# Optimization experiments

Measured on AMD Instinct MI355X. Metric: run time of the kernel, lower is better.

The kernel has to match this reference:

```python
import jax, jax.numpy as jnp
import numpy as np

B, N, K = 32, 2048, 16          # graphs, nodes per graph, knn neighbors
F_IN, F_OUT, P = 32, 64, 3      # feature dims, pos dim


def setup_inputs() -> dict:
    key = jax.random.key(0)
    ks = jax.random.split(key, 6)
    x = jax.random.normal(ks[0], (B * N, F_IN), dtype=jnp.float32)
    pos = jax.random.normal(ks[1], (B * N, P), dtype=jnp.float32)
    # contiguous equal-size graphs: batch[i] = i // N
    batch = (jnp.arange(B * N, dtype=jnp.int32) // N).astype(jnp.int32)
    W_edge = jax.random.normal(ks[2], (2 * F_IN, F_OUT), dtype=jnp.float32) * 0.1
    b_edge = jax.random.normal(ks[3], (F_OUT,), dtype=jnp.float32) * 0.1
    W_nn = jax.random.normal(ks[4], (F_IN, F_OUT), dtype=jnp.float32) * 0.1
    b_nn = jax.random.normal(ks[5], (F_OUT,), dtype=jnp.float32) * 0.1
    return {"x": x, "pos": pos, "W_edge": W_edge, "b_edge": b_edge,
            "W_nn": W_nn, "b_nn": b_nn, "batch": batch}


def reference(x, pos, W_edge, b_edge, W_nn, b_nn, batch):
    # batch is contiguous with N nodes per graph -> reshape to [B, N, .]
    xb = x.reshape(B, N, F_IN)
    pb = pos.reshape(B, N, P)

    # --- knn_graph on pos, per graph (flow='source_to_target') ---
    sq = jnp.sum(pb * pb, axis=-1)                                   # [B, N]
    d2 = sq[:, :, None] + sq[:, None, :] - 2.0 * jnp.einsum('bnd,bmd->bnm', pb, pb)
    d2 = d2 + jnp.eye(N, dtype=d2.dtype) * 1e30                      # exclude self-loops
    _, idx = jax.lax.top_k(-d2, K)                                   # idx[b, i, k] = k-th nearest j of i

    # --- EdgeConv: message = edge_nn(concat(x_i, x_j - x_i)), aggr=max at i ---
    x_j = jnp.take_along_axis(xb, idx.reshape(B, N * K, 1), axis=1).reshape(B, N, K, F_IN)
    x_i = xb[:, :, None, :]                                          # [B, N, 1, F_IN]
    msg = jnp.concatenate([jnp.broadcast_to(x_i, (B, N, K, F_IN)), x_j - x_i], axis=-1)
    h = jax.nn.relu(msg @ W_edge + b_edge)                           # [B, N, K, F_OUT]
    edge_out = jnp.max(h, axis=2)                                    # max-aggregate over neighbors

    # --- skip branch: nn(x) ---
    skip = jax.nn.relu(xb @ W_nn + b_nn)                             # [B, N, F_OUT]

    return (edge_out + skip).reshape(B * N, F_OUT)
```

## Files before the change

kernel.cpp:

```cpp
#include <hip/hip_runtime.h>

#define NB     32
#define NPTS   2048
#define KNN    16
#define FIN    32
#define FOUT   64

typedef __attribute__((ext_vector_type(8))) short bf16x8;
typedef __attribute__((ext_vector_type(4))) float f32x4;

__device__ inline unsigned bf16pk(float lo, float hi) {
    unsigned a = __float_as_uint(lo), b = __float_as_uint(hi);
    a = (a + 0x7fffu + ((a >> 16) & 1u)) >> 16;
    b = (b + 0x7fffu + ((b >> 16) & 1u)) >> 16;
    return (a & 0xffffu) | (b << 16);
}


#define CEA(x, y) { float _t = fminf(x, y); y = fmaxf(x, y); x = _t; }
#define CED(x, y) { float _t = fmaxf(x, y); y = fminf(x, y); x = _t; }

#define BMERGE16(dk) \
    CEA(dk[0],dk[8])  CEA(dk[1],dk[9])  CEA(dk[2],dk[10]) CEA(dk[3],dk[11]) \
    CEA(dk[4],dk[12]) CEA(dk[5],dk[13]) CEA(dk[6],dk[14]) CEA(dk[7],dk[15]) \
    CEA(dk[0],dk[4])  CEA(dk[1],dk[5])  CEA(dk[2],dk[6])  CEA(dk[3],dk[7])  \
    CEA(dk[8],dk[12]) CEA(dk[9],dk[13]) CEA(dk[10],dk[14]) CEA(dk[11],dk[15]) \
    CEA(dk[0],dk[2])  CEA(dk[1],dk[3])  CEA(dk[4],dk[6])  CEA(dk[5],dk[7])  \
    CEA(dk[8],dk[10]) CEA(dk[9],dk[11]) CEA(dk[12],dk[14]) CEA(dk[13],dk[15]) \
    CEA(dk[0],dk[1])  CEA(dk[2],dk[3])  CEA(dk[4],dk[5])  CEA(dk[6],dk[7])  \
    CEA(dk[8],dk[9])  CEA(dk[10],dk[11]) CEA(dk[12],dk[13]) CEA(dk[14],dk[15])

#define NET8(a) \
    CED(a[0],a[1]) CED(a[2],a[3]) CED(a[4],a[5]) CED(a[6],a[7]) \
    CED(a[0],a[2]) CED(a[1],a[3]) CED(a[4],a[6]) CED(a[5],a[7]) \
    CED(a[1],a[2]) CED(a[5],a[6]) \
    CED(a[0],a[4]) CED(a[1],a[5]) CED(a[2],a[6]) CED(a[3],a[7]) \
    CED(a[2],a[4]) CED(a[3],a[5]) \
    CED(a[1],a[2]) CED(a[3],a[4]) CED(a[5],a[6])

__global__ __launch_bounds__(256) void sq_kernel(
    const float* __restrict__ pos, float4* __restrict__ P4)
{
    const int i = blockIdx.x * 256 + threadIdx.x;
    const float px = pos[i*3 + 0];
    const float py = pos[i*3 + 1];
    const float pz = pos[i*3 + 2];
    const float sq = __fadd_rn(__fadd_rn(__fmul_rn(px,px), __fmul_rn(py,py)),
                               __fmul_rn(pz,pz));
    P4[i] = make_float4(px, py, pz, sq);
}

#define CH   8
#define CHL  (NPTS / CH)

#define D2P(C, DST)                                                        \
    {                                                                      \
        float _dot = __fmaf_rn(me.z, (C).z,                                \
                      __fmaf_rn(me.y, (C).y, __fmul_rn(me.x, (C).x)));     \
        DST = __fmaf_rn(-2.0f, _dot, (C).w);                               \
    }

#define SBATCH2(JB, EXCLF)                                                 \
    {                                                                      \
        float a[8], a2[8];                                                 \
        _Pragma("unroll")                                                  \
        for (int i = 0; i < 8; ++i) {                                      \
            const int j = (JB) + i;                                        \
            const float4 c = pb4[j];                                       \
            float d2;                                                      \
            D2P(c, d2)                                                     \
            a[i] = (EXCLF && j == q) ? 1e30f : d2;                         \
        }                                                                  \
        _Pragma("unroll")                                                  \
        for (int i = 0; i < 8; ++i) {                                      \
            const int j = (JB) + 8 + i;                                    \
            const float4 c = pb4[j];                                       \
            float d2;                                                      \
            D2P(c, d2)                                                     \
            a2[i] = (EXCLF && j == q) ? 1e30f : d2;                        \
        }                                                                  \
        NET8(a)                                                            \
        NET8(a2)                                                           \
        _Pragma("unroll")                                                  \
        for (int i = 0; i < 8; ++i) dk[8+i] = fminf(dk[8+i], a[i]);        \
        BMERGE16(dk)                                                       \
        _Pragma("unroll")                                                  \
        for (int i = 0; i < 8; ++i) dk[8+i] = fminf(dk[8+i], a2[i]);       \
        BMERGE16(dk)                                                       \
    }

#define APP(DD, JJ)                                                        \
    if ((DD) <= tthr) {                                                    \
        if ((DD) < tthr) {                                                 \
            if (cntS + cntT >= KNN) --cntT;                                \
            JL[base + cntS * 64 + l] = (JJ);                               \
            ++cntS;                                                        \
        } else if (cntS + cntT < KNN) {                                    \
            JL[base + (KNN - 1 - cntT) * 64 + l] = (JJ);                   \
            ++cntT;                                                        \
        }                                                                  \
    }

#define RESC(JJ, EXCLF)                                                    \
    {                                                                      \
        const float4 c = pb4[(JJ)];                                        \
        float d2;                                                          \
        D2P(c, d2)                                                         \
        if (EXCLF && (JJ) == q) d2 = 1e30f;                                \
        APP(d2, (JJ))                                                      \
    }

#define ESTRIDE 66
#define IDXS    17

__global__ __launch_bounds__(512, 8) void knn_mlp_kernel(
    const float4* __restrict__ P4, const float* __restrict__ x,
    const float* __restrict__ W_edge, const float* __restrict__ b_edge,
    const float* __restrict__ W_nn,   const float* __restrict__ b_nn,
    float* __restrict__ out)
{
    __shared__ __attribute__((aligned(16))) char smem[39168];
    float* V    = (float*)smem;
    int*   CNTS = (int*)(smem + 32768);
    int*   IDX  = (int*)(smem + 34816);

    const int orig = blockIdx.x;
    const int b    = ((orig & 7) << 2) | ((orig >> 3) & 3);
    const int slab = orig >> 5;
    const int t    = threadIdx.x;
    const int w    = __builtin_amdgcn_readfirstlane(t >> 6);
    const int l    = t & 63;

    const float4* __restrict__ pb4 = P4 + (size_t)b * NPTS;
    const int    q  = slab * 64 + l;
    const float4 me = pb4[q];

    {
        float dk[KNN];
        #pragma unroll
        for (int s = 0; s < KNN; ++s) dk[s] = 1e30f;

        const int j0  = w * CHL;
        const int exw = slab >> 2;
        const int lo  = j0 + (slab & 3) * 64;

        if (w == exw) {
            for (int jb = j0;      jb < lo;        jb += 16) SBATCH2(jb, false)
            for (int jb = lo;      jb < lo + 64;   jb += 16) SBATCH2(jb, true)
            for (int jb = lo + 64; jb < j0 + CHL;  jb += 16) SBATCH2(jb, false)
        } else {
            for (int jb = j0;      jb < j0 + CHL;  jb += 16) SBATCH2(jb, false)
        }

        #pragma unroll
        for (int s = 0; s < KNN; ++s)
            V[(w * KNN + s) * 64 + l] = dk[s];
        __syncthreads();

        for (int c2 = 0; c2 < CH; ++c2) {
            if (c2 == w) continue;
            float v[KNN];
            #pragma unroll
            for (int s2 = 0; s2 < KNN; ++s2)
                v[s2] = V[(c2 * KNN + s2) * 64 + l];
            #pragma unroll
            for (int s = 0; s < KNN; ++s) dk[s] = fminf(dk[s], v[KNN-1-s]);
            BMERGE16(dk)
        }
        const float tthr = dk[KNN-1];
        __syncthreads();

        int* JL = (int*)V;
        const int base = w * KNN * 64;
        int cntS = 0, cntT = 0;
        if (w == exw) {
            for (int j = j0;      j < lo;        ++j) RESC(j, false)
            for (int j = lo;      j < lo + 64;   ++j) RESC(j, true)
            for (int j = lo + 64; j < j0 + CHL;  ++j) RESC(j, false)
        } else {
            for (int j = j0;      j < j0 + CHL;  ++j) RESC(j, false)
        }
        CNTS[w * 64 + l] = cntS | (cntT << 16);
        __syncthreads();

        if (w == 0) {
            int outc = 0;
            for (int c2 = 0; c2 < CH; ++c2) {
                int cs = CNTS[c2 * 64 + l] & 0xffff;
                for (int s2 = 0; s2 < cs && outc < KNN; ++s2)
                    IDX[l * IDXS + outc++] = JL[(c2 * KNN + s2) * 64 + l];
            }
            for (int c2 = 0; c2 < CH && outc < KNN; ++c2) {
                int ct = CNTS[c2 * 64 + l] >> 16;
                for (int s2 = 0; s2 < ct && outc < KNN; ++s2)
                    IDX[l * IDXS + outc++] =
                        JL[(c2 * KNN + (KNN - 1 - s2)) * 64 + l];
            }
        }
        __syncthreads();
    }

    const int c15 = l & 15;
    const int g   = l >> 4;
    const int nbase = b * NPTS + slab * 64;
    const int gbase = b * NPTS;

    float* E = (float*)smem;
    float* S = (float*)(smem + 16896);

    const f32x4 zf = {0.f, 0.f, 0.f, 0.f};

    {
        const int ng = w & 3;
        const int f0 = (w >> 2) * 2;

        const float* rp = x + (size_t)(nbase + ng * 16 + c15) * FIN + g * 8;
        float4 v0 = *(const float4*)rp;
        float4 v1 = *(const float4*)(rp + 4);
        int4 pk = make_int4(bf16pk(v0.x, v0.y), bf16pk(v0.z, v0.w),
                            bf16pk(v1.x, v1.y), bf16pk(v1.z, v1.w));
        bf16x8 afi = *(bf16x8*)&pk;

        #pragma unroll
        for (int ff = 0; ff < 2; ++ff) {
            const int col = 16 * (f0 + ff) + c15;
            unsigned pd[4], pn[4];
            #pragma unroll
            for (int d = 0; d < 4; ++d) {
                const int k0 = g * 8 + 2 * d;
                float h0 = W_edge[(FIN + k0)     * FOUT + col];
                float h1 = W_edge[(FIN + k0 + 1) * FOUT + col];
                pd[d] = bf16pk(W_edge[k0       * FOUT + col] - h0,
                               W_edge[(k0 + 1) * FOUT + col] - h1);
                pn[d] = bf16pk(W_nn[k0 * FOUT + col], W_nn[(k0+1) * FOUT + col]);
            }
            int4 bd = make_int4(pd[0], pd[1], pd[2], pd[3]);
            int4 bn = make_int4(pn[0], pn[1], pn[2], pn[3]);
            f32x4 baseF = __builtin_amdgcn_mfma_f32_16x16x32_bf16(
                afi, *(bf16x8*)&bd, zf, 0, 0, 0);
            f32x4 skipF = __builtin_amdgcn_mfma_f32_16x16x32_bf16(
                afi, *(bf16x8*)&bn, zf, 0, 0, 0);
            const float be  = b_edge[col];
            const float bnn = b_nn[col];
            #pragma unroll
            for (int reg = 0; reg < 4; ++reg) {
                const int nd = ng * 16 + g * 4 + reg;
                E[nd * ESTRIDE + col] = baseF[reg] + be;
                S[nd * ESTRIDE + col] = fmaxf(skipF[reg] + bnn, 0.f);
            }
        }
    }
    __syncthreads();

    {
        const int n0l = w * 8;

        int4 Bhi[4];
        #pragma unroll
        for (int ff = 0; ff < 4; ++ff) {
            const int col = 16 * ff + c15;
            unsigned ph[4];
            #pragma unroll
            for (int d = 0; d < 4; ++d) {
                const int k0 = g * 8 + 2 * d;
                ph[d] = bf16pk(W_edge[(FIN + k0)     * FOUT + col],
                               W_edge[(FIN + k0 + 1) * FOUT + col]);
            }
            Bhi[ff] = make_int4(ph[0], ph[1], ph[2], ph[3]);
        }

        int nbA = IDX[(n0l + 0) * IDXS + c15];
        int nbB = IDX[(n0l + 1) * IDXS + c15];
        const float* rpA = x + (size_t)(gbase + nbA) * FIN + g * 8;
        const float* rpB = x + (size_t)(gbase + nbB) * FIN + g * 8;
        float4 Aa = *(const float4*)rpA, Ab = *(const float4*)(rpA + 4);
        float4 Ba = *(const float4*)rpB, Bb = *(const float4*)(rpB + 4);

        #pragma unroll 1
        for (int i = 0; i < 8; i += 2) {
            float4 c0 = Aa, c1 = Ab;
            if (i + 2 < 8) {
                int nb = IDX[(n0l + i + 2) * IDXS + c15];
                const float* rp2 = x + (size_t)(gbase + nb) * FIN + g * 8;
                Aa = *(const float4*)rp2;
                Ab = *(const float4*)(rp2 + 4);
            }
            {
                int4 pk2 = make_int4(bf16pk(c0.x, c0.y), bf16pk(c0.z, c0.w),
                                     bf16pk(c1.x, c1.y), bf16pk(c1.z, c1.w));
                bf16x8 af = *(bf16x8*)&pk2;
                float rmax[4];
                #pragma unroll
                for (int ff = 0; ff < 4; ++ff) {
                    f32x4 z = __builtin_amdgcn_mfma_f32_16x16x32_bf16(
                        af, *(bf16x8*)&Bhi[ff], zf, 0, 0, 0);
                    float m = fmaxf(fmaxf(z[0], z[1]), fmaxf(z[2], z[3]));
                    m = fmaxf(m, __shfl_xor(m, 16));
                    m = fmaxf(m, __shfl_xor(m, 32));
                    rmax[ff] = m;
                }
                float val = (g == 0) ? rmax[0] : (g == 1) ? rmax[1]
                          : (g == 2) ? rmax[2] : rmax[3];
                const int nd = n0l + i;
                float e = fmaxf(val + E[nd * ESTRIDE + g * 16 + c15], 0.f);
                float s = S[nd * ESTRIDE + g * 16 + c15];
                out[(size_t)(nbase + nd) * FOUT + g * 16 + c15] = e + s;
            }

            float4 d0 = Ba, d1 = Bb;
            if (i + 3 < 8) {
                int nb = IDX[(n0l + i + 3) * IDXS + c15];
                const float* rp2 = x + (size_t)(gbase + nb) * FIN + g * 8;
                Ba = *(const float4*)rp2;
                Bb = *(const float4*)(rp2 + 4);
            }
            {
                int4 pk2 = make_int4(bf16pk(d0.x, d0.y), bf16pk(d0.z, d0.w),
                                     bf16pk(d1.x, d1.y), bf16pk(d1.z, d1.w));
                bf16x8 af = *(bf16x8*)&pk2;
                float rmax[4];
                #pragma unroll
                for (int ff = 0; ff < 4; ++ff) {
                    f32x4 z = __builtin_amdgcn_mfma_f32_16x16x32_bf16(
                        af, *(bf16x8*)&Bhi[ff], zf, 0, 0, 0);
                    float m = fmaxf(fmaxf(z[0], z[1]), fmaxf(z[2], z[3]));
                    m = fmaxf(m, __shfl_xor(m, 16));
                    m = fmaxf(m, __shfl_xor(m, 32));
                    rmax[ff] = m;
                }
                float val = (g == 0) ? rmax[0] : (g == 1) ? rmax[1]
                          : (g == 2) ? rmax[2] : rmax[3];
                const int nd = n0l + i + 1;
                float e = fmaxf(val + E[nd * ESTRIDE + g * 16 + c15], 0.f);
                float s = S[nd * ESTRIDE + g * 16 + c15];
                out[(size_t)(nbase + nd) * FOUT + g * 16 + c15] = e + s;
            }
        }
    }
}

extern "C" void kernel_launch(void* const* d_in, const int* in_sizes, int n_in,
                              void* d_out, int out_size, void* d_ws, size_t ws_size,
                              hipStream_t stream) {
    const float* x      = (const float*)d_in[0];
    const float* pos    = (const float*)d_in[1];
    const float* W_edge = (const float*)d_in[2];
    const float* b_edge = (const float*)d_in[3];
    const float* W_nn   = (const float*)d_in[4];
    const float* b_nn   = (const float*)d_in[5];

    float4* P4   = (float4*)d_ws;
    float*  outp = (float*)d_out;

    sq_kernel     <<<NB * NPTS / 256, 256, 0, stream>>>(pos, P4);
    knn_mlp_kernel<<<NB * 32,         512, 0, stream>>>(P4, x, W_edge, b_edge,
                                                        W_nn, b_nn, outp);
}
```

Baseline: 196.2 us.

## Software-pipeline candidate loads in KNN scans and parallelize index compaction across waves

Both the top-k scan and the rescan loop now prefetch the next 16 candidate positions into registers while the current batch is being processed, and the three-segment self-exclusion loops are merged into one uniform loop with a predicated check. The serial compaction of neighbor indices, previously done by wave 0 alone, is replaced by a per-wave prefix-sum placement so all 8 waves write their survivors in parallel. This is meant to hide global/L2 load latency and remove a serialized tail, at the cost of 16 extra float4 registers per thread, which may lower occupancy under the 512x8 launch bounds.

```diff
diff --git a/kernel.cpp b/kernel.cpp
--- a/kernel.cpp
+++ b/kernel.cpp
@@ -60,35 +60,6 @@
         DST = __fmaf_rn(-2.0f, _dot, (C).w);                               \
     }
 
-#define SBATCH2(JB, EXCLF)                                                 \
-    {                                                                      \
-        float a[8], a2[8];                                                 \
-        _Pragma("unroll")                                                  \
-        for (int i = 0; i < 8; ++i) {                                      \
-            const int j = (JB) + i;                                        \
-            const float4 c = pb4[j];                                       \
-            float d2;                                                      \
-            D2P(c, d2)                                                     \
-            a[i] = (EXCLF && j == q) ? 1e30f : d2;                         \
-        }                                                                  \
-        _Pragma("unroll")                                                  \
-        for (int i = 0; i < 8; ++i) {                                      \
-            const int j = (JB) + 8 + i;                                    \
-            const float4 c = pb4[j];                                       \
-            float d2;                                                      \
-            D2P(c, d2)                                                     \
-            a2[i] = (EXCLF && j == q) ? 1e30f : d2;                        \
-        }                                                                  \
-        NET8(a)                                                            \
-        NET8(a2)                                                           \
-        _Pragma("unroll")                                                  \
-        for (int i = 0; i < 8; ++i) dk[8+i] = fminf(dk[8+i], a[i]);        \
-        BMERGE16(dk)                                                       \
-        _Pragma("unroll")                                                  \
-        for (int i = 0; i < 8; ++i) dk[8+i] = fminf(dk[8+i], a2[i]);       \
-        BMERGE16(dk)                                                       \
-    }
-
 #define APP(DD, JJ)                                                        \
     if ((DD) <= tthr) {                                                    \
         if ((DD) < tthr) {                                                 \
@@ -101,15 +72,6 @@
         }                                                                  \
     }
 
-#define RESC(JJ, EXCLF)                                                    \
-    {                                                                      \
-        const float4 c = pb4[(JJ)];                                        \
-        float d2;                                                          \
-        D2P(c, d2)                                                         \
-        if (EXCLF && (JJ) == q) d2 = 1e30f;                                \
-        APP(d2, (JJ))                                                      \
-    }
-
 #define ESTRIDE 66
 #define IDXS    17
 
@@ -135,21 +97,51 @@
     const int    q  = slab * 64 + l;
     const float4 me = pb4[q];
 
+    const int  j0  = w * CHL;
+    const int  exw = slab >> 2;
+    const bool ex  = (w == exw);
+
+    int* JL = (int*)V;
+    const int base = w * KNN * 64;
+    int cntS = 0, cntT = 0;
+
     {
         float dk[KNN];
         #pragma unroll
         for (int s = 0; s < KNN; ++s) dk[s] = 1e30f;
 
-        const int j0  = w * CHL;
-        const int exw = slab >> 2;
-        const int lo  = j0 + (slab & 3) * 64;
-
-        if (w == exw) {
-            for (int jb = j0;      jb < lo;        jb += 16) SBATCH2(jb, false)
-            for (int jb = lo;      jb < lo + 64;   jb += 16) SBATCH2(jb, true)
-            for (int jb = lo + 64; jb < j0 + CHL;  jb += 16) SBATCH2(jb, false)
-        } else {
-            for (int jb = j0;      jb < j0 + CHL;  jb += 16) SBATCH2(jb, false)
+        {
+            float4 cur[16];
+            #pragma unroll
+            for (int i = 0; i < 16; ++i) cur[i] = pb4[j0 + i];
+
+            for (int jb = j0; jb < j0 + CHL; jb += 16) {
+                float a[8], a2[8];
+                #pragma unroll
+                for (int i = 0; i < 8; ++i) {
+                    float d2;
+                    D2P(cur[i], d2)
+                    a[i] = (ex && (jb + i) == q) ? 1e30f : d2;
+                }
+                #pragma unroll
+                for (int i = 0; i < 8; ++i) {
+                    float d2;
+                    D2P(cur[8 + i], d2)
+                    a2[i] = (ex && (jb + 8 + i) == q) ? 1e30f : d2;
+                }
+                const int pjb = (jb + 16 < j0 + CHL) ? (jb + 16) : j0;
+                #pragma unroll
+                for (int i = 0; i < 16; ++i) cur[i] = pb4[pjb + i];
+
+                NET8(a)
+                NET8(a2)
+                #pragma unroll
+                for (int i = 0; i < 8; ++i) dk[8+i] = fminf(dk[8+i], a[i]);
+                BMERGE16(dk)
+                #pragma unroll
+                for (int i = 0; i < 8; ++i) dk[8+i] = fminf(dk[8+i], a2[i]);
+                BMERGE16(dk)
+            }
         }
 
         #pragma unroll
@@ -170,35 +162,51 @@
         const float tthr = dk[KNN-1];
         __syncthreads();
 
-        int* JL = (int*)V;
-        const int base = w * KNN * 64;
-        int cntS = 0, cntT = 0;
-        if (w == exw) {
-            for (int j = j0;      j < lo;        ++j) RESC(j, false)
-            for (int j = lo;      j < lo + 64;   ++j) RESC(j, true)
-            for (int j = lo + 64; j < j0 + CHL;  ++j) RESC(j, false)
-        } else {
-            for (int j = j0;      j < j0 + CHL;  ++j) RESC(j, false)
+        {
+            float4 cur[16];
+            #pragma unroll
+            for (int i = 0; i < 16; ++i) cur[i] = pb4[j0 + i];
+
+            for (int jb = j0; jb < j0 + CHL; jb += 16) {
+                float dd[16];
+                #pragma unroll
+                for (int i = 0; i < 16; ++i) {
+                    float d2;
+                    D2P(cur[i], d2)
+                    dd[i] = (ex && (jb + i) == q) ? 1e30f : d2;
+                }
+                const int pjb = (jb + 16 < j0 + CHL) ? (jb + 16) : j0;
+                #pragma unroll
+                for (int i = 0; i < 16; ++i) cur[i] = pb4[pjb + i];
+
+                #pragma unroll
+                for (int i = 0; i < 16; ++i) { APP(dd[i], jb + i) }
+            }
         }
         CNTS[w * 64 + l] = cntS | (cntT << 16);
         __syncthreads();
-
-        if (w == 0) {
-            int outc = 0;
-            for (int c2 = 0; c2 < CH; ++c2) {
-                int cs = CNTS[c2 * 64 + l] & 0xffff;
-                for (int s2 = 0; s2 < cs && outc < KNN; ++s2)
-                    IDX[l * IDXS + outc++] = JL[(c2 * KNN + s2) * 64 + l];
-            }
-            for (int c2 = 0; c2 < CH && outc < KNN; ++c2) {
-                int ct = CNTS[c2 * 64 + l] >> 16;
-                for (int s2 = 0; s2 < ct && outc < KNN; ++s2)
-                    IDX[l * IDXS + outc++] =
-                        JL[(c2 * KNN + (KNN - 1 - s2)) * 64 + l];
-            }
-        }
-        __syncthreads();
-    }
+    }
+
+    {
+        int pS = 0, pT = 0, totS = 0;
+        #pragma unroll
+        for (int c2 = 0; c2 < CH; ++c2) {
+            int cc = CNTS[c2 * 64 + l];
+            int cs = cc & 0xffff, ct = cc >> 16;
+            if (c2 < w) { pS += cs; pT += ct; }
+            totS += cs;
+        }
+        for (int s2 = 0; s2 < cntS; ++s2) {
+            int pos = pS + s2;
+            if (pos < KNN) IDX[l * IDXS + pos] = JL[base + s2 * 64 + l];
+        }
+        for (int s2 = 0; s2 < cntT; ++s2) {
+            int pos = totS + pT + s2;
+            if (pos < KNN)
+                IDX[l * IDXS + pos] = JL[base + (KNN - 1 - s2) * 64 + l];
+        }
+    }
+    __syncthreads();
 
     const int c15 = l & 15;
     const int g   = l >> 4;
```

Result: slower. 251.3 us (+28.1%).
